# Performance work log

Hardware: AMD Instinct MI355X
Metric: run time of the kernel (lower is better)

The kernel has to match this reference:

```python
import jax, jax.numpy as jnp
import numpy as np

NUM_HEADS = 16

def setup_inputs() -> dict:
    key = jax.random.key(0)
    ks = jax.random.split(key, 5)
    B, T, C = 2, 2048, 1024
    s = 0.02
    return {
        "x": jax.random.normal(ks[0], (B, T, C), dtype=jnp.float32),
        "in_w": jax.random.normal(ks[1], (3 * C, C), dtype=jnp.float32) * s,
        "in_b": jax.random.normal(ks[2], (3 * C,), dtype=jnp.float32) * s,
        "out_w": jax.random.normal(ks[3], (C, C), dtype=jnp.float32) * s,
        "out_b": jax.random.normal(ks[4], (C,), dtype=jnp.float32) * s,
    }

def reference(x, in_w, in_b, out_w, out_b):
    B, T, C = x.shape
    H = NUM_HEADS
    D = C // H
    qvk = x @ in_w.T + in_b  # (B, T, 3C)
    # einops 'b t (d k h) -> k b h t d': factor 3C as (D, 3, H), D outermost
    qvk = qvk.reshape(B, T, D, 3, H).transpose(3, 0, 4, 1, 2)  # (3, B, H, T, D)
    q, v, k = qvk[0], qvk[1], qvk[2]  # note q, v, k assignment order
    scores = jnp.einsum('bhid,bhjd->bhij', q, k) * (D ** -0.5)  # (B, H, T, T)
    causal = jnp.tril(jnp.ones((T, T), dtype=bool))
    scores = jnp.where(causal, scores, -jnp.inf)
    attn = jax.nn.softmax(scores, axis=-1)
    out = jnp.einsum('bhij,bhjd->bhid', attn, v)  # (B, H, T, D)
    out = out.transpose(0, 2, 1, 3).reshape(B, T, C)  # 'b h t d -> b t (h d)'
    return out @ out_w.T + out_b
```

## Files before the change

### kernel.cpp

```cpp
#include <hip/hip_runtime.h>


#define BB 2
#define TT 2048
#define CC 1024
#define HH 16
#define DD 64
#define MM (BB*TT)
#define N3 (3*CC)
#define BH (BB*HH)

typedef unsigned short u16;
typedef unsigned int   u32;
typedef __bf16 bf16x8 __attribute__((ext_vector_type(8)));
typedef float  f32x4  __attribute__((ext_vector_type(4)));

__device__ __forceinline__ u16 f32_to_bf16(float f) {
  u32 u = __float_as_uint(f);
  return (u16)((u + 0x7fffu + ((u >> 16) & 1u)) >> 16);
}
__device__ __forceinline__ u16 f32_to_bf16_fast(float f) {
  return (u16)((__float_as_uint(f) + 0x8000u) >> 16);
}
__device__ __forceinline__ u32 pack2_bf16(float a, float b) {
  u32 ua = __float_as_uint(a) + 0x8000u;
  u32 ub = __float_as_uint(b) + 0x8000u;
  return __builtin_amdgcn_perm(ub, ua, 0x07060302);
}

#define N4_X  (MM * CC / 4)
#define N4_W  (N3 * CC / 4)
#define N4_OW (CC * CC / 4)
__global__ __launch_bounds__(256) void cast_all(const float* __restrict__ x,
                                                const float* __restrict__ in_w,
                                                const float* __restrict__ out_w,
                                                u16* __restrict__ xb,
                                                u16* __restrict__ wb,
                                                u16* __restrict__ owb) {
  int i = blockIdx.x * 256 + threadIdx.x;
  const float* src; u16* dst; int j;
  if (i < N4_X)            { src = x;     dst = xb;  j = i; }
  else if (i < N4_X + N4_W){ src = in_w;  dst = wb;  j = i - N4_X; }
  else                     { src = out_w; dst = owb; j = i - N4_X - N4_W; }
  float4 f = reinterpret_cast<const float4*>(src)[j];
  uint2 pk;
  pk.x = (u32)f32_to_bf16(f.x) | ((u32)f32_to_bf16(f.y) << 16);
  pk.y = (u32)f32_to_bf16(f.z) | ((u32)f32_to_bf16(f.w) << 16);
  reinterpret_cast<uint2*>(dst)[j] = pk;
}

__device__ __forceinline__ void gemm_core(const u16* __restrict__ Ag,
                                          const u16* __restrict__ Bg,
                                          int K, u16* Al, u16* Bl,
                                          int m0, int n0, f32x4 acc[4][4]) {
  const int tid = threadIdx.x, lane = tid & 63, w = tid >> 6;
  const int quad = lane >> 4, colr = lane & 15;
  const int mw = (w >> 1) * 64, nw = (w & 1) * 64;
  const int srow = lane >> 3, scol = lane & 7;
  const uint4* Al4 = reinterpret_cast<const uint4*>(Al);
  const uint4* Bl4 = reinterpret_cast<const uint4*>(Bl);
  for (int kt = 0; kt < K / 64; ++kt) {
    __syncthreads();
    #pragma unroll
    for (int ii = 0; ii < 4; ++ii) {
      int inst = w * 4 + ii;
      int row = inst * 8 + srow;
      int cs = scol ^ (row & 7);
      const u16* ga = Ag + (size_t)(m0 + row) * K + kt * 64 + cs * 8;
      const u16* gb = Bg + (size_t)(n0 + row) * K + kt * 64 + cs * 8;
      __builtin_amdgcn_global_load_lds(
          (const __attribute__((address_space(1))) void*)ga,
          (__attribute__((address_space(3))) void*)(Al + inst * 512), 16, 0, 0);
      __builtin_amdgcn_global_load_lds(
          (const __attribute__((address_space(1))) void*)gb,
          (__attribute__((address_space(3))) void*)(Bl + inst * 512), 16, 0, 0);
    }
    __syncthreads();
    #pragma unroll
    for (int ks = 0; ks < 2; ++ks) {
      bf16x8 af[4], bfr[4];
      #pragma unroll
      for (int t = 0; t < 4; ++t) {
        int mrow = mw + t * 16 + colr;
        af[t]  = __builtin_bit_cast(bf16x8, Al4[mrow * 8 + ((ks * 4 + quad) ^ (mrow & 7))]);
        int nrow = nw + t * 16 + colr;
        bfr[t] = __builtin_bit_cast(bf16x8, Bl4[nrow * 8 + ((ks * 4 + quad) ^ (nrow & 7))]);
      }
      #pragma unroll
      for (int mt = 0; mt < 4; ++mt)
        #pragma unroll
        for (int nt = 0; nt < 4; ++nt)
          acc[mt][nt] = __builtin_amdgcn_mfma_f32_16x16x32_bf16(af[mt], bfr[nt], acc[mt][nt], 0, 0, 0);
    }
  }
}

__global__ __launch_bounds__(256) void gemm_qkv(const u16* __restrict__ xb,
                                                const u16* __restrict__ wb,
                                                const float* __restrict__ in_b,
                                                u16* __restrict__ Y) {
  __shared__ __align__(16) u16 Al[128 * 64];
  __shared__ __align__(16) u16 Bl[128 * 64];
  const int lane = threadIdx.x & 63, w = threadIdx.x >> 6;
  const int quad = lane >> 4, colr = lane & 15;
  const int mw = (w >> 1) * 64, nw = (w & 1) * 64;
  const int m0 = blockIdx.x * 128, n0 = blockIdx.y * 128;
  f32x4 acc[4][4];
  #pragma unroll
  for (int mt = 0; mt < 4; ++mt)
    #pragma unroll
    for (int nt = 0; nt < 4; ++nt) acc[mt][nt] = (f32x4){0.f, 0.f, 0.f, 0.f};
  gemm_core(xb, wb, CC, Al, Bl, m0, n0, acc);
  float bias[4];
  #pragma unroll
  for (int nt = 0; nt < 4; ++nt) bias[nt] = in_b[n0 + nw + nt * 16 + colr];
  #pragma unroll
  for (int mt = 0; mt < 4; ++mt)
    #pragma unroll
    for (int e = 0; e < 4; ++e) {
      int row = m0 + mw + mt * 16 + quad * 4 + e;
      #pragma unroll
      for (int nt = 0; nt < 4; ++nt)
        Y[(size_t)row * N3 + n0 + nw + nt * 16 + colr] = f32_to_bf16(acc[mt][nt][e] + bias[nt]);
    }
}

__global__ __launch_bounds__(256) void repack_qkv(const u16* __restrict__ Y,
                                                  u16* __restrict__ qkv) {
  __shared__ __align__(16) u16 Yl[N3];
  const int m = blockIdx.x, tid = threadIdx.x;
  const int b_ = m >> 11, t = m & (TT - 1);
  const uint4* Yg = reinterpret_cast<const uint4*>(Y + (size_t)m * N3);
  uint4* Yl4 = reinterpret_cast<uint4*>(Yl);
  for (int i = tid; i < N3 / 8; i += 256) Yl4[i] = Yg[i];
  __syncthreads();
  for (int it = tid; it < 768; it += 256) {
    int h = it & 15, s = (it >> 4) % 3, dg = it / 48;
    int col = s * 16 + h;
    u32 lo = (u32)Yl[(dg * 4 + 0) * 48 + col] | ((u32)Yl[(dg * 4 + 1) * 48 + col] << 16);
    u32 hi = (u32)Yl[(dg * 4 + 2) * 48 + col] | ((u32)Yl[(dg * 4 + 3) * 48 + col] << 16);
    uint2 pk; pk.x = lo; pk.y = hi;
    size_t base = (((size_t)s * BH + b_ * HH + h) * TT + t) * DD + dg * 4;
    *reinterpret_cast<uint2*>(qkv + base) = pk;
  }
}

__global__ __launch_bounds__(128) void attn_mfma(const u16* __restrict__ qkv,
                                                 u16* __restrict__ aout) {
  __shared__ __align__(16) u32   Vt[2][64 * 36];
  __shared__ __align__(16) float Pl[2 * 32 * 68];
  const int tid  = threadIdx.x;
  const int lane = tid & 63, w = tid >> 6;
  const int quad = lane >> 4, colr = lane & 15;
  const int flat = blockIdx.x;
  const int bh = (flat & 7) * 4 + (flat >> 7);
  const int pr = (flat >> 3) & 15;
  const int b_ = bh >> 4, h = bh & 15;

  const uint4* Qg4 = reinterpret_cast<const uint4*>(qkv + (size_t)bh * TT * DD);
  const uint4* Vg4 = reinterpret_cast<const uint4*>(qkv + ((size_t)BH + bh) * TT * DD);
  const uint4* Kg4 = reinterpret_cast<const uint4*>(qkv + ((size_t)2 * BH + bh) * TT * DD);
  const float4* Pl4 = reinterpret_cast<const float4*>(Pl);

  const int s_jp = tid & 31, s_half = tid >> 5;
  const int wbase = w * (32 * 68);

  for (int pass = 0; pass < 2; ++pass) {
    const int qt = pass ? (31 - pr) : pr;
    const int i0 = qt * 64;
    const int jmax = qt;

    bf16x8 qa[2][2];
    #pragma unroll
    for (int u = 0; u < 2; ++u)
      #pragma unroll
      for (int ks = 0; ks < 2; ++ks)
        qa[u][ks] = __builtin_bit_cast(bf16x8,
            Qg4[(size_t)(i0 + w * 32 + u * 16 + colr) * 8 + ks * 4 + quad]);

    f32x4 oacc[2][4];
    #pragma unroll
    for (int u = 0; u < 2; ++u)
      #pragma unroll
      for (int dt = 0; dt < 4; ++dt) oacc[u][dt] = (f32x4){0.f, 0.f, 0.f, 0.f};
    float lp[2] = {0.f, 0.f};

    uint4 va[2], vb[2];
    #pragma unroll
    for (int io = 0; io < 2; ++io) {
      va[io] = Vg4[(size_t)(2 * s_jp) * 8 + s_half + io * 4];
      vb[io] = Vg4[(size_t)(2 * s_jp + 1) * 8 + s_half + io * 4];
    }

    for (int jt = 0; jt <= jmax; ++jt) {
      const int j0 = jt * 64;
      u32* vtw = Vt[jt & 1];
      const uint4* vt4 = reinterpret_cast<const uint4*>(Vt[jt & 1]);

      uint4 kraw[4][2];
      #pragma unroll
      for (int t4 = 0; t4 < 4; ++t4)
        #pragma unroll
        for (int ks = 0; ks < 2; ++ks)
          kraw[t4][ks] = Kg4[(size_t)(j0 + t4 * 16 + colr) * 8 + ks * 4 + quad];

      #pragma unroll
      for (int io = 0; io < 2; ++io) {
        const int oc = s_half + io * 4;
        u32 aw[4] = {va[io].x, va[io].y, va[io].z, va[io].w};
        u32 bw[4] = {vb[io].x, vb[io].y, vb[io].z, vb[io].w};
        #pragma unroll
        for (int m = 0; m < 4; ++m) {
          vtw[(oc * 8 + 2 * m)     * 36 + s_jp] = __builtin_amdgcn_perm(bw[m], aw[m], 0x05040100);
          vtw[(oc * 8 + 2 * m + 1) * 36 + s_jp] = __builtin_amdgcn_perm(bw[m], aw[m], 0x07060302);
        }
      }
      if (jt < jmax) {
        int nj = j0 + 64;
        #pragma unroll
        for (int io = 0; io < 2; ++io) {
          va[io] = Vg4[(size_t)(nj + 2 * s_jp) * 8 + s_half + io * 4];
          vb[io] = Vg4[(size_t)(nj + 2 * s_jp + 1) * 8 + s_half + io * 4];
        }
      }
      __syncthreads();

      f32x4 sacc[2][4];
      #pragma unroll
      for (int u = 0; u < 2; ++u)
        #pragma unroll
        for (int t4 = 0; t4 < 4; ++t4) sacc[u][t4] = (f32x4){0.f, 0.f, 0.f, 0.f};
      #pragma unroll
      for (int t4 = 0; t4 < 4; ++t4)
        #pragma unroll
        for (int ks = 0; ks < 2; ++ks) {
          bf16x8 kb = __builtin_bit_cast(bf16x8, kraw[t4][ks]);
          #pragma unroll
          for (int u = 0; u < 2; ++u)
            sacc[u][t4] = __builtin_amdgcn_mfma_f32_16x16x32_bf16(qa[u][ks], kb, sacc[u][t4], 0, 0, 0);
        }

      const bool maskt = (jt == qt);
      #pragma unroll
      for (int u = 0; u < 2; ++u)
        #pragma unroll
        for (int t4 = 0; t4 < 4; ++t4)
          #pragma unroll
          for (int rg = 0; rg < 4; ++rg) {
            float p = __builtin_amdgcn_exp2f(sacc[u][t4][rg] * 0.18033688011112042f);
            if (maskt && (t4 * 16 + colr > w * 32 + u * 16 + quad * 4 + rg)) p = 0.f;
            Pl[wbase + (u * 16 + quad * 4 + rg) * 68 + t4 * 16 + colr] = p;
          }

      bf16x8 pa[2][2];
      #pragma unroll
      for (int u = 0; u < 2; ++u)
        #pragma unroll
        for (int ks = 0; ks < 2; ++ks) {
          int b4 = (wbase + (u * 16 + colr) * 68 + ks * 32 + quad * 8) >> 2;
          float4 f0 = Pl4[b4], f1 = Pl4[b4 + 1];
          lp[u] += ((f0.x + f0.y) + (f0.z + f0.w)) + ((f1.x + f1.y) + (f1.z + f1.w));
          uint4 up;
          up.x = pack2_bf16(f0.x, f0.y); up.y = pack2_bf16(f0.z, f0.w);
          up.z = pack2_bf16(f1.x, f1.y); up.w = pack2_bf16(f1.z, f1.w);
          pa[u][ks] = __builtin_bit_cast(bf16x8, up);
        }

      #pragma unroll
      for (int dt = 0; dt < 4; ++dt)
        #pragma unroll
        for (int ks = 0; ks < 2; ++ks) {
          bf16x8 vfr = __builtin_bit_cast(bf16x8, vt4[(dt * 16 + colr) * 9 + ks * 4 + quad]);
          #pragma unroll
          for (int u = 0; u < 2; ++u)
            oacc[u][dt] = __builtin_amdgcn_mfma_f32_16x16x32_bf16(pa[u][ks], vfr, oacc[u][dt], 0, 0, 0);
        }
    }

    #pragma unroll
    for (int u = 0; u < 2; ++u) {
      float ls = lp[u];
      ls += __shfl_xor(ls, 16);
      ls += __shfl_xor(ls, 32);
      float linv[4];
      #pragma unroll
      for (int rg = 0; rg < 4; ++rg)
        linv[rg] = 1.0f / __shfl(ls, quad * 4 + rg);
      #pragma unroll
      for (int dt = 0; dt < 4; ++dt)
        #pragma unroll
        for (int rg = 0; rg < 4; ++rg) {
          int ig = i0 + w * 32 + u * 16 + quad * 4 + rg;
          size_t off = ((size_t)(b_ * TT + ig)) * CC + h * DD + dt * 16 + colr;
          aout[off] = f32_to_bf16_fast(oacc[u][dt][rg] * linv[rg]);
        }
    }
    __syncthreads();
  }
}

__global__ __launch_bounds__(256) void gemm_out(const u16* __restrict__ ab,
                                                const u16* __restrict__ owb,
                                                const float* __restrict__ out_b,
                                                float* __restrict__ out) {
  __shared__ __align__(16) u16 Al[128 * 64];
  __shared__ __align__(16) u16 Bl[128 * 64];
  const int lane = threadIdx.x & 63, w = threadIdx.x >> 6;
  const int quad = lane >> 4, colr = lane & 15;
  const int mw = (w >> 1) * 64, nw = (w & 1) * 64;
  const int m0 = blockIdx.x * 128, n0 = blockIdx.y * 128;
  f32x4 acc[4][4];
  #pragma unroll
  for (int mt = 0; mt < 4; ++mt)
    #pragma unroll
    for (int nt = 0; nt < 4; ++nt) acc[mt][nt] = (f32x4){0.f, 0.f, 0.f, 0.f};
  gemm_core(ab, owb, CC, Al, Bl, m0, n0, acc);
  float bias[4];
  #pragma unroll
  for (int nt = 0; nt < 4; ++nt) bias[nt] = out_b[n0 + nw + nt * 16 + colr];
  #pragma unroll
  for (int mt = 0; mt < 4; ++mt)
    #pragma unroll
    for (int e = 0; e < 4; ++e) {
      int row = m0 + mw + mt * 16 + quad * 4 + e;
      #pragma unroll
      for (int nt = 0; nt < 4; ++nt)
        out[(size_t)row * CC + n0 + nw + nt * 16 + colr] = acc[mt][nt][e] + bias[nt];
    }
}

extern "C" void kernel_launch(void* const* d_in, const int* in_sizes, int n_in,
                              void* d_out, int out_size, void* d_ws, size_t ws_size,
                              hipStream_t stream) {
  const float* x     = (const float*)d_in[0];
  const float* in_w  = (const float*)d_in[1];
  const float* in_b  = (const float*)d_in[2];
  const float* out_w = (const float*)d_in[3];
  const float* out_b = (const float*)d_in[4];
  float* out = (float*)d_out;

  char* ws = (char*)d_ws;
  u16* xb  = (u16*)(ws + 0);
  u16* ab  = (u16*)(ws + 0);
  u16* wb  = (u16*)(ws + 8388608);
  u16* owb = (u16*)(ws + 14680064);
  u16* Y   = (u16*)(ws + 16777216);
  u16* qkv = (u16*)(ws + 41943040);

  cast_all<<<dim3((N4_X + N4_W + N4_OW) / 256), 256, 0, stream>>>(x, in_w, out_w, xb, wb, owb);

  gemm_qkv<<<dim3(MM / 128, N3 / 128), 256, 0, stream>>>(xb, wb, in_b, Y);
  repack_qkv<<<dim3(MM), 256, 0, stream>>>(Y, qkv);
  attn_mfma<<<dim3(512), 128, 0, stream>>>(qkv, ab);
  gemm_out<<<dim3(MM / 128, CC / 128), 256, 0, stream>>>(ab, owb, out_b, out);
}
```

Before: 226.2 us.

## Split long causal attention rows across two blocks with partial-sum finalize

Doubles the attention grid so each block handles a balanced share of key tiles. The long upper query tile's key range is split between two blocks that write unnormalized partial outputs and row sums to workspace. A new finalize kernel adds the two partials, normalizes and writes bf16. The aim is better load balance and more blocks in flight on the GPU. The cost is an extra kernel launch and fp32 partial traffic through global memory, and summing partials without a max rescale assumes the softmax is computed without a running max.

```diff
diff --git a/kernel.cpp b/kernel.cpp
--- a/kernel.cpp
+++ b/kernel.cpp
@@ -145,17 +145,21 @@
   }
 }
 
-__global__ __launch_bounds__(128) void attn_mfma(const u16* __restrict__ qkv,
-                                                 u16* __restrict__ aout) {
+__global__ __launch_bounds__(128, 2) void attn_mfma(const u16* __restrict__ qkv,
+                                                    u16* __restrict__ aout,
+                                                    float* __restrict__ po,
+                                                    float* __restrict__ pl) {
   __shared__ __align__(16) u32   Vt[2][64 * 36];
   __shared__ __align__(16) float Pl[2 * 32 * 68];
   const int tid  = threadIdx.x;
   const int lane = tid & 63, w = tid >> 6;
   const int quad = lane >> 4, colr = lane & 15;
   const int flat = blockIdx.x;
-  const int bh = (flat & 7) * 4 + (flat >> 7);
-  const int pr = (flat >> 3) & 15;
+  const int hf = (flat >> 3) & 1;
+  const int pr = (flat >> 4) & 15;
+  const int bh = (flat & 7) * 4 + (flat >> 8);
   const int b_ = bh >> 4, h = bh & 15;
+  const int slot = (((bh << 4) + pr) << 1) | hf;
 
   const uint4* Qg4 = reinterpret_cast<const uint4*>(qkv + (size_t)bh * TT * DD);
   const uint4* Vg4 = reinterpret_cast<const uint4*>(qkv + ((size_t)BH + bh) * TT * DD);
@@ -165,10 +169,13 @@
   const int s_jp = tid & 31, s_half = tid >> 5;
   const int wbase = w * (32 * 68);
 
-  for (int pass = 0; pass < 2; ++pass) {
-    const int qt = pass ? (31 - pr) : pr;
+  const int nseg = 2 - hf;
+  for (int seg = 0; seg < nseg; ++seg) {
+    const bool final_out = (hf == 0) && (seg == 0);
+    const int qt  = final_out ? pr : (31 - pr);
+    const int jlo = (hf == 1) ? (16 - pr) : 0;
+    const int jhi = (hf == 1) ? (31 - pr) : (seg == 0 ? pr : 15 - pr);
     const int i0 = qt * 64;
-    const int jmax = qt;
 
     bf16x8 qa[2][2];
     #pragma unroll
@@ -188,11 +195,11 @@
     uint4 va[2], vb[2];
     #pragma unroll
     for (int io = 0; io < 2; ++io) {
-      va[io] = Vg4[(size_t)(2 * s_jp) * 8 + s_half + io * 4];
-      vb[io] = Vg4[(size_t)(2 * s_jp + 1) * 8 + s_half + io * 4];
-    }
-
-    for (int jt = 0; jt <= jmax; ++jt) {
+      va[io] = Vg4[(size_t)(jlo * 64 + 2 * s_jp) * 8 + s_half + io * 4];
+      vb[io] = Vg4[(size_t)(jlo * 64 + 2 * s_jp + 1) * 8 + s_half + io * 4];
+    }
+
+    for (int jt = jlo; jt <= jhi; ++jt) {
       const int j0 = jt * 64;
       u32* vtw = Vt[jt & 1];
       const uint4* vt4 = reinterpret_cast<const uint4*>(Vt[jt & 1]);
@@ -215,7 +222,7 @@
           vtw[(oc * 8 + 2 * m + 1) * 36 + s_jp] = __builtin_amdgcn_perm(bw[m], aw[m], 0x07060302);
         }
       }
-      if (jt < jmax) {
+      if (jt < jhi) {
         int nj = j0 + 64;
         #pragma unroll
         for (int io = 0; io < 2; ++io) {
@@ -282,20 +289,55 @@
       float ls = lp[u];
       ls += __shfl_xor(ls, 16);
       ls += __shfl_xor(ls, 32);
-      float linv[4];
-      #pragma unroll
-      for (int rg = 0; rg < 4; ++rg)
-        linv[rg] = 1.0f / __shfl(ls, quad * 4 + rg);
-      #pragma unroll
-      for (int dt = 0; dt < 4; ++dt)
-        #pragma unroll
-        for (int rg = 0; rg < 4; ++rg) {
-          int ig = i0 + w * 32 + u * 16 + quad * 4 + rg;
-          size_t off = ((size_t)(b_ * TT + ig)) * CC + h * DD + dt * 16 + colr;
-          aout[off] = f32_to_bf16_fast(oacc[u][dt][rg] * linv[rg]);
-        }
+      if (final_out) {
+        float linv[4];
+        #pragma unroll
+        for (int rg = 0; rg < 4; ++rg)
+          linv[rg] = 1.0f / __shfl(ls, quad * 4 + rg);
+        #pragma unroll
+        for (int dt = 0; dt < 4; ++dt)
+          #pragma unroll
+          for (int rg = 0; rg < 4; ++rg) {
+            int ig = i0 + w * 32 + u * 16 + quad * 4 + rg;
+            size_t off = ((size_t)(b_ * TT + ig)) * CC + h * DD + dt * 16 + colr;
+            aout[off] = f32_to_bf16_fast(oacc[u][dt][rg] * linv[rg]);
+          }
+      } else {
+        float* ob = po + (size_t)slot * 4096;
+        #pragma unroll
+        for (int dt = 0; dt < 4; ++dt)
+          #pragma unroll
+          for (int rg = 0; rg < 4; ++rg)
+            ob[(w * 32 + u * 16 + quad * 4 + rg) * 64 + dt * 16 + colr] = oacc[u][dt][rg];
+        if (lane < 16) pl[slot * 64 + w * 32 + u * 16 + lane] = ls;
+      }
     }
     __syncthreads();
+  }
+}
+
+__global__ __launch_bounds__(256) void attn_finalize(const float* __restrict__ po,
+                                                     const float* __restrict__ pl,
+                                                     u16* __restrict__ aout) {
+  const int blk = blockIdx.x;
+  const int bh = blk >> 4, pr = blk & 15;
+  const int qt = 31 - pr;
+  const int b_ = bh >> 4, h = bh & 15;
+  const int t = threadIdx.x;
+  const int r = t >> 2, dq = t & 3;
+  const size_t s0 = (size_t)blk * 2, s1 = s0 + 1;
+  const float4* o0 = reinterpret_cast<const float4*>(po + s0 * 4096 + r * 64 + dq * 16);
+  const float4* o1 = reinterpret_cast<const float4*>(po + s1 * 4096 + r * 64 + dq * 16);
+  float inv = 1.0f / (pl[s0 * 64 + r] + pl[s1 * 64 + r]);
+  int ig = qt * 64 + r;
+  u16* dst = aout + ((size_t)(b_ * TT + ig)) * CC + h * DD + dq * 16;
+  #pragma unroll
+  for (int c = 0; c < 4; ++c) {
+    float4 a = o0[c], b = o1[c];
+    uint2 pk;
+    pk.x = pack2_bf16((a.x + b.x) * inv, (a.y + b.y) * inv);
+    pk.y = pack2_bf16((a.z + b.z) * inv, (a.w + b.w) * inv);
+    *reinterpret_cast<uint2*>(dst + c * 4) = pk;
   }
 }
 
@@ -345,12 +387,15 @@
   u16* wb  = (u16*)(ws + 8388608);
   u16* owb = (u16*)(ws + 14680064);
   u16* Y   = (u16*)(ws + 16777216);
+  float* po = (float*)(ws + 16777216);
+  float* pl = (float*)(ws + 16777216 + 16777216);
   u16* qkv = (u16*)(ws + 41943040);
 
   cast_all<<<dim3((N4_X + N4_W + N4_OW) / 256), 256, 0, stream>>>(x, in_w, out_w, xb, wb, owb);
 
   gemm_qkv<<<dim3(MM / 128, N3 / 128), 256, 0, stream>>>(xb, wb, in_b, Y);
   repack_qkv<<<dim3(MM), 256, 0, stream>>>(Y, qkv);
-  attn_mfma<<<dim3(512), 128, 0, stream>>>(qkv, ab);
+  attn_mfma<<<dim3(1024), 128, 0, stream>>>(qkv, ab, po, pl);
+  attn_finalize<<<dim3(512), 256, 0, stream>>>(po, pl, ab);
   gemm_out<<<dim3(MM / 128, CC / 128), 256, 0, stream>>>(ab, owb, out_b, out);
 }
```

Measured after the change: 223.3 us. No clear change (-1.3%).
